# Optimization experiments

Hardware: AMD Instinct MI355X
Metric: run time of the kernel (lower is better)

Reference implementation:

```python
import jax, jax.numpy as jnp
import numpy as np

D_MODEL = 256; N_HEADS = 8; N_LEVELS = 4; N_POINTS = 4; NUM_ITER = 2
SHAPES = [(92, 160), (46, 80), (23, 40), (12, 20)]  # 4-level FPN, Len_in = 19560
LEN_IN = sum(h * w for h, w in SHAPES)
N_BATCH = 2


def _offset_bias():
    # faithful to _reset_parameters grid init of sampling_offsets.bias
    thetas = jnp.arange(N_HEADS, dtype=jnp.float32) * (2.0 * np.pi / N_HEADS)
    grid = jnp.stack([jnp.cos(thetas), jnp.sin(thetas)], -1)
    grid = grid / jnp.max(jnp.abs(grid), axis=-1, keepdims=True)
    grid = jnp.tile(grid[:, None, None, :], (1, N_LEVELS, N_POINTS, 1))
    grid = grid * (jnp.arange(N_POINTS, dtype=jnp.float32) + 1.0)[None, None, :, None]
    return grid.reshape(-1)


def setup_inputs() -> dict:
    key = jax.random.key(0)
    ks = jax.random.split(key, 12)
    N, Lq, d = N_BATCH, LEN_IN, D_MODEL
    s = 0.02
    return {
        "query0": jax.random.normal(ks[0], (N, Lq, d), jnp.float32),
        "query1": jax.random.normal(ks[1], (N, Lq, d), jnp.float32),
        "reference_points": jax.random.uniform(ks[2], (N, Lq, N_LEVELS, 2), jnp.float32),
        "input_flatten0": jax.random.normal(ks[3], (N, LEN_IN, d), jnp.float32),
        "input_flatten1": jax.random.normal(ks[4], (N, LEN_IN, d), jnp.float32),
        "input_spatial_shapes": jnp.array(SHAPES, jnp.int32),
        "input_level_start_index": jnp.array(np.cumsum([0] + [h * w for h, w in SHAPES[:-1]]), jnp.int32),
        "W_so": s * jax.random.normal(ks[5], (d, N_HEADS * N_LEVELS * N_POINTS * 2), jnp.float32),
        "b_so": _offset_bias(),
        "W_aw": s * jax.random.normal(ks[6], (d, N_HEADS * N_LEVELS * N_POINTS), jnp.float32),
        "b_aw": jnp.zeros((N_HEADS * N_LEVELS * N_POINTS,), jnp.float32),
        "W_v": s * jax.random.normal(ks[7], (d, d), jnp.float32),
        "b_v": jnp.zeros((d,), jnp.float32),
        "W_o": s * jax.random.normal(ks[8], (d, d), jnp.float32),
        "b_o": jnp.zeros((d,), jnp.float32),
        "W_agg": s * jax.random.normal(ks[9], (d * NUM_ITER, d), jnp.float32),
        "b_agg": jnp.zeros((d,), jnp.float32),
    }


def _sample_level(v_l, loc_l, H, W):
    # v_l: (N, nH, H*W, D); loc_l: (N, Lq, nH, P, 2) in [0,1]
    # bilinear, align_corners=False, zero padding (matches grid_sample fallback / CUDA kernel)
    x = loc_l[..., 0] * W - 0.5
    y = loc_l[..., 1] * H - 0.5
    x0 = jnp.floor(x); y0 = jnp.floor(y)

    def gather(xi, yi):
        inb = ((xi >= 0) & (xi <= W - 1) & (yi >= 0) & (yi <= H - 1)).astype(v_l.dtype)
        idx = (jnp.clip(yi, 0, H - 1) * W + jnp.clip(xi, 0, W - 1)).astype(jnp.int32)
        idx_t = jnp.transpose(idx, (0, 2, 1, 3))  # (N, nH, Lq, P)
        g = jax.vmap(jax.vmap(lambda vt, it: vt[it]))(v_l, idx_t)  # (N, nH, Lq, P, D)
        return g * jnp.transpose(inb, (0, 2, 1, 3))[..., None]

    def wt(w):
        return jnp.transpose(w, (0, 2, 1, 3))[..., None]

    return (wt((y0 + 1 - y) * (x0 + 1 - x)) * gather(x0, y0)
            + wt((y0 + 1 - y) * (x - x0)) * gather(x0 + 1, y0)
            + wt((y - y0) * (x0 + 1 - x)) * gather(x0, y0 + 1)
            + wt((y - y0) * (x - x0)) * gather(x0 + 1, y0 + 1))  # (N, nH, Lq, P, D)


def _ms_deform_attn(value, loc, attn, shapes, starts):
    # value: (N, Len_in, nH, D); loc: (N, Lq, nH, L, P, 2); attn: (N, Lq, nH, L, P)
    v = jnp.transpose(value, (0, 2, 1, 3))  # (N, nH, Len_in, D)
    acc = None
    for lvl in range(N_LEVELS):
        H, W = int(shapes[lvl, 0]), int(shapes[lvl, 1])
        s = int(starts[lvl])
        out_l = _sample_level(v[:, :, s:s + H * W], loc[:, :, :, lvl], H, W)
        a = jnp.transpose(attn[:, :, :, lvl], (0, 2, 1, 3))  # (N, nH, Lq, P)
        term = jnp.einsum('nhqpd,nhqp->nhqd', out_l, a)
        acc = term if acc is None else acc + term
    N, nH, Lq, D = acc.shape
    return jnp.transpose(acc, (0, 2, 1, 3)).reshape(N, Lq, nH * D)


def reference(query0, query1, reference_points, input_flatten0, input_flatten1,
              input_spatial_shapes, input_level_start_index,
              W_so, b_so, W_aw, b_aw, W_v, b_v, W_o, b_o, W_agg, b_agg):
    shapes = np.asarray(input_spatial_shapes)
    starts = np.asarray(input_level_start_index)
    N, Lq, d = query0.shape
    nH, L, P = N_HEADS, N_LEVELS, N_POINTS
    queries = [query0, query1]
    flats = [input_flatten0, input_flatten1]
    values, offs, aws = [], [], []
    for q, f in zip(queries, flats):
        values.append((f @ W_v + b_v).reshape(N, -1, nH, d // nH))
        offs.append((q @ W_so + b_so).reshape(N, Lq, nH, L, P, 2))
        aws.append((q @ W_aw + b_aw).reshape(N, Lq, nH, L * P))
    # joint softmax over num_iter * n_levels * n_points (the one-shot trick)
    aw_all = jax.nn.softmax(jnp.concatenate(aws, axis=-1), axis=-1)
    # (L, 2) normalizer = (W, H)
    normalizer = jnp.stack([input_spatial_shapes[..., 1], input_spatial_shapes[..., 0]], -1).astype(query0.dtype)
    outs = []
    for i in range(NUM_ITER):
        aw_i = aw_all[..., i * L * P:(i + 1) * L * P].reshape(N, Lq, nH, L, P)
        loc = reference_points[:, :, None, :, None, :] + offs[i] / normalizer[None, None, None, :, None, :]
        o = _ms_deform_attn(values[i], loc, aw_i, shapes, starts)
        outs.append(o @ W_o + b_o)
    return jnp.concatenate(outs, axis=-1) @ W_agg + b_agg
```

## Files before the change

kernel.cpp:

```cpp
#include <hip/hip_runtime.h>
#include <math.h>

#define NBATCH 2
#define LQ     19560
#define LEN    19560
#define NQ     (NBATCH * LQ)
#define DMODEL 256
#define NHEADS 8
#define HDIM   32
#define NLEV   4
#define NPTS   4
#define LDQS   384

typedef __bf16 bf16x8 __attribute__((ext_vector_type(8)));
typedef float  f32x4  __attribute__((ext_vector_type(4)));
typedef float  f32x2  __attribute__((ext_vector_type(2)));

__device__ inline unsigned short f2bf(float f) {
    unsigned int u = __float_as_uint(f);
    u += 0x7FFFu + ((u >> 16) & 1u);
    return (unsigned short)(u >> 16);
}
__device__ inline f32x2 bfpair(unsigned int u) {
    f32x2 r;
    r.x = __uint_as_float(u << 16);
    r.y = __uint_as_float(u & 0xFFFF0000u);
    return r;
}

__global__ __launch_bounds__(256) void prep_all(
    const float* __restrict__ q0, const float* __restrict__ q1,
    const float* __restrict__ f0, const float* __restrict__ f1,
    const float* __restrict__ Wv, const float* __restrict__ Wso,
    const float* __restrict__ Waw, const float* __restrict__ bso,
    const float* __restrict__ baw,
    const float* __restrict__ Wo, const float* __restrict__ Wagg,
    const float* __restrict__ bo, const float* __restrict__ bagg,
    unsigned short* __restrict__ Qb0, unsigned short* __restrict__ Qb1,
    unsigned short* __restrict__ Fb0, unsigned short* __restrict__ Fb1,
    unsigned short* __restrict__ Wvt, unsigned short* __restrict__ Wsoawt,
    float* __restrict__ bsoaw,
    unsigned short* __restrict__ Wfcat, float* __restrict__ bfused)
{
    const int b = blockIdx.x;
    if (b < 19560) {
        const int tsel = b / 4890;
        const int x = b - tsel * 4890;
        const float* s = (tsel & 2) ? ((tsel & 1) ? f1 : f0) : ((tsel & 1) ? q1 : q0);
        unsigned short* d = (tsel & 2) ? ((tsel & 1) ? Fb1 : Fb0) : ((tsel & 1) ? Qb1 : Qb0);
        size_t i = ((size_t)x * 256 + threadIdx.x) * 8;
        float4 a = *(const float4*)(s + i);
        float4 c = *(const float4*)(s + i + 4);
        union { uint4 u; unsigned short h[8]; } t;
        t.h[0] = f2bf(a.x); t.h[1] = f2bf(a.y); t.h[2] = f2bf(a.z); t.h[3] = f2bf(a.w);
        t.h[4] = f2bf(c.x); t.h[5] = f2bf(c.y); t.h[6] = f2bf(c.z); t.h[7] = f2bf(c.w);
        if (tsel & 2) {
            *(uint4*)(d + i) = t.u;
        } else {
            size_t row = i >> 8; int c8 = (int)(i & 255);
            *(uint4*)(d + row * 768 + 512 + c8) = t.u;
        }
    } else if (b < 19560 + 640) {
        int o = (b - 19560) * 256 + threadIdx.x;
        if (o < 65536) {
            int n = o >> 8, k = o & 255;
            Wvt[o] = f2bf(Wv[(size_t)k * 256 + n]);
        } else {
            int p = o - 65536;
            int n = p >> 8, k = p & 255;
            float v = (n < 256) ? Wso[(size_t)k * 256 + n] : Waw[(size_t)k * 128 + (n - 256)];
            Wsoawt[p] = f2bf(v);
        }
        if (o < 384) bsoaw[o] = (o < 256) ? bso[o] : baw[o - 256];
    } else {
        int k = b - 20200;
        int n = threadIdx.x;
        float s0 = 0.f, s1 = 0.f;
        for (int j = 0; j < 256; j++) {
            float w = Wo[k * 256 + j];
            s0 += w * Wagg[j * 256 + n];
            s1 += w * Wagg[(256 + j) * 256 + n];
        }
        Wfcat[(size_t)n * 512 + k]       = f2bf(s0);
        Wfcat[(size_t)n * 512 + 256 + k] = f2bf(s1);
        if (k == 0) {
            float bb = bagg[n];
            for (int j = 0; j < 256; j++)
                bb += bo[j] * (Wagg[j * 256 + n] + Wagg[(256 + j) * 256 + n]);
            bfused[n] = bb;
        }
    }
}

__global__ __launch_bounds__(256) void gemm_mega(
    const unsigned short* __restrict__ Qa0, const unsigned short* __restrict__ Qa1,
    const unsigned short* __restrict__ Fb0, const unsigned short* __restrict__ Fb1,
    const unsigned short* __restrict__ Wsoawt, const unsigned short* __restrict__ Wvt,
    const float* __restrict__ bsoaw, const float* __restrict__ bv,
    float* __restrict__ QS0, float* __restrict__ QS1,
    unsigned short* __restrict__ V0, unsigned short* __restrict__ V1,
    float* __restrict__ AW0, float* __restrict__ AW1, int awld, int zbase)
{
    const int z = blockIdx.z + zbase;
    const int isVal = (z >= 2 && z < 4);
    const int isLog = (z >= 4);
    if (isLog && blockIdx.x != 0) return;
    const int zz = z & 1;

    __shared__ __align__(16) unsigned short As[128 * 64];
    __shared__ __align__(16) unsigned short Bs[128 * 64];

    const unsigned short* A = isVal ? (zz ? Fb1 : Fb0) : (zz ? Qa1 : Qa0);
    const unsigned short* Bt = isVal ? Wvt : Wsoawt;
    const float* bias = isVal ? bv : bsoaw;
    const int lda = isVal ? 256 : 768;
    const int btrow0 = isLog ? 256 : 0;
    const int bias0 = btrow0;

    const int tid  = threadIdx.x;
    const int w    = tid >> 6, lane = tid & 63;
    const int wm = w >> 1, wn = w & 1;
    const int m0 = blockIdx.y * 128, n0 = blockIdx.x * 128;
    const int lr = lane & 15, quad = lane >> 4;

    const int sr  = lane >> 3;
    const int scl = (lane & 7) ^ sr;
    const int colb = scl * 8;
    size_t arow[4], brow[4];
    #pragma unroll
    for (int j = 0; j < 4; j++) {
        int r = (w * 4 + j) * 8 + sr;
        int ra = m0 + r; if (ra > NQ - 1) ra = NQ - 1;
        arow[j] = (size_t)ra * lda;
        brow[j] = (size_t)(btrow0 + n0 + r) * 256;
    }

    const f32x4 zero = {0.f, 0.f, 0.f, 0.f};
    f32x4 acc[4][4];
    #pragma unroll
    for (int i = 0; i < 4; i++)
        #pragma unroll
        for (int j = 0; j < 4; j++) acc[i][j] = zero;

    for (int t = 0; t < 256; t += 64) {
        #pragma unroll
        for (int j = 0; j < 4; j++) {
            int lofs = __builtin_amdgcn_readfirstlane((w * 4 + j) * 1024);
            __builtin_amdgcn_global_load_lds(
                (const __attribute__((address_space(1))) void*)(A + arow[j] + t + colb),
                (__attribute__((address_space(3))) void*)((char*)As + lofs), 16, 0, 0);
            __builtin_amdgcn_global_load_lds(
                (const __attribute__((address_space(1))) void*)(Bt + brow[j] + t + colb),
                (__attribute__((address_space(3))) void*)((char*)Bs + lofs), 16, 0, 0);
        }
        __syncthreads();

        #pragma unroll
        for (int kk = 0; kk < 2; kk++) {
            bf16x8 af[4], bff[4];
            #pragma unroll
            for (int mi = 0; mi < 4; mi++) {
                int R = wm * 64 + mi * 16 + lr;
                int pc = ((kk * 4 + quad) ^ (lr & 7)) * 16;
                af[mi] = *(const bf16x8*)((const char*)As + R * 128 + pc);
            }
            #pragma unroll
            for (int ni = 0; ni < 4; ni++) {
                int R = wn * 64 + ni * 16 + lr;
                int pc = ((kk * 4 + quad) ^ (lr & 7)) * 16;
                bff[ni] = *(const bf16x8*)((const char*)Bs + R * 128 + pc);
            }
            #pragma unroll
            for (int mi = 0; mi < 4; mi++)
                #pragma unroll
                for (int ni = 0; ni < 4; ni++)
                    acc[mi][ni] = __builtin_amdgcn_mfma_f32_16x16x32_bf16(
                        af[mi], bff[ni], acc[mi][ni], 0, 0, 0);
        }
        __syncthreads();
    }

    float* Cf = isLog ? (zz ? AW1 : AW0) : (zz ? QS1 : QS0);
    const int ldc = isLog ? awld : LDQS;
    unsigned short* Cb = zz ? V1 : V0;
    #pragma unroll
    for (int mi = 0; mi < 4; mi++) {
        #pragma unroll
        for (int reg = 0; reg < 4; reg++) {
            int row = m0 + wm * 64 + mi * 16 + quad * 4 + reg;
            if (row >= NQ) continue;
            #pragma unroll
            for (int ni = 0; ni < 4; ni++) {
                int col = n0 + wn * 64 + ni * 16 + lr;
                float v = acc[mi][ni][reg] + bias[bias0 + col];
                if (!isVal) {
                    Cf[(size_t)row * ldc + col] = v;
                } else {
                    int n = row >= LQ ? 1 : 0;
                    int pos = row - n * LQ;
                    int h = col >> 5, d = col & 31;
                    Cb[((size_t)(n * NHEADS + h) * LEN + pos) * HDIM + d] = f2bf(v);
                }
            }
        }
    }
}

#define QCHUNK 64
#define CHUNKS ((LQ + QCHUNK - 1) / QCHUNK)

__global__ __launch_bounds__(256) void ms_sample(
    const unsigned short* __restrict__ V0, const unsigned short* __restrict__ V1,
    const float* __restrict__ QS0, const float* __restrict__ QS1,
    const float* __restrict__ AW0, const float* __restrict__ AW1, int awld,
    const float* __restrict__ refp, unsigned short* __restrict__ Ocat)
{
    __shared__ unsigned int Sidx[16][65][4];
    __shared__ float        Swt [16][65][4];

    const int b = blockIdx.x;
    const int h = b & 7;
    const int rest = b >> 3;
    const int chunk = rest % CHUNKS;
    const int inn   = rest / CHUNKS;
    const int n  = inn & 1;
    const int it = inn >> 1;

    const int tid = threadIdx.x;
    const int ql  = tid >> 2;
    const int lj  = tid & 3;
    const int qraw = chunk * QCHUNK + ql;
    const bool valid = qraw < LQ;
    const int q  = valid ? qraw : LQ - 1;
    const int nq = n * LQ + q;

    const unsigned short* __restrict__ val = it ? V1 : V0;
    const float* __restrict__ QS = it ? QS1 : QS0;
    const unsigned short* __restrict__ vb2 =
        val + (size_t)(n * NHEADS + h) * LEN * HDIM;

    const int Hs[4] = {92, 46, 23, 12};
    const int Ws[4] = {160, 80, 40, 20};
    const int Ss[4] = {0, 14720, 18400, 19320};

    const float* prow = QS + (size_t)nq * LDQS;

    {
        const float4 l0 = *(const float4*)(AW0 + (size_t)nq * awld + (h << 4) + lj * 4);
        const float4 l1 = *(const float4*)(AW1 + (size_t)nq * awld + (h << 4) + lj * 4);
        float m = fmaxf(fmaxf(fmaxf(l0.x, l0.y), fmaxf(l0.z, l0.w)),
                        fmaxf(fmaxf(l1.x, l1.y), fmaxf(l1.z, l1.w)));
        m = fmaxf(m, __shfl_xor(m, 1));
        m = fmaxf(m, __shfl_xor(m, 2));
        float e0x = expf(l0.x - m), e0y = expf(l0.y - m);
        float e0z = expf(l0.z - m), e0w = expf(l0.w - m);
        float e1x = expf(l1.x - m), e1y = expf(l1.y - m);
        float e1z = expf(l1.z - m), e1w = expf(l1.w - m);
        float s = ((e0x + e0y) + (e0z + e0w)) + ((e1x + e1y) + (e1z + e1w));
        s += __shfl_xor(s, 1);
        s += __shfl_xor(s, 2);
        const float inv = 1.0f / s;
        float avs[4];
        if (it) { avs[0] = e1x * inv; avs[1] = e1y * inv; avs[2] = e1z * inv; avs[3] = e1w * inv; }
        else    { avs[0] = e0x * inv; avs[1] = e0y * inv; avs[2] = e0z * inv; avs[3] = e0w * inv; }

        const int H = Hs[lj], W = Ws[lj], S = Ss[lj];
        const float4 o0 = *(const float4*)(prow + (h << 5) + lj * 8);
        const float4 o1 = *(const float4*)(prow + (h << 5) + lj * 8 + 4);
        const float2 rp = *(const float2*)(refp + (size_t)nq * 8 + lj * 2);
        const float fx = rp.x * (float)W - 0.5f;
        const float fy = rp.y * (float)H - 0.5f;
        const float oxs[4] = {o0.x, o0.z, o1.x, o1.z};
        const float oys[4] = {o0.y, o0.w, o1.y, o1.w};
        #pragma unroll
        for (int k = 0; k < NPTS; k++) {
            const float x = fx + oxs[k];
            const float y = fy + oys[k];
            const float x0f = floorf(x), y0f = floorf(y);
            const int x0 = (int)x0f, y0 = (int)y0f;
            const float wx1 = x - x0f, wy1 = y - y0f;
            const float wx0 = 1.0f - wx1, wy0 = 1.0f - wy1;
            const int xc0 = min(max(x0, 0), W - 1);
            const int xc1 = min(max(x0 + 1, 0), W - 1);
            const int yc0 = min(max(y0, 0), H - 1);
            const int yc1 = min(max(y0 + 1, 0), H - 1);
            const float a = avs[k];
            const float ay0 = ((unsigned int)y0 < (unsigned int)H) ? a * wy0 : 0.f;
            const float ay1 = ((unsigned int)(y0 + 1) < (unsigned int)H) ? a * wy1 : 0.f;
            const float mx0 = ((unsigned int)x0 < (unsigned int)W) ? wx0 : 0.f;
            const float mx1 = ((unsigned int)(x0 + 1) < (unsigned int)W) ? wx1 : 0.f;
            const int r0 = S + yc0 * W, r1 = S + yc1 * W;
            uint4 eo4;
            eo4.x = (unsigned int)(r0 + xc0) << 5;
            eo4.y = (unsigned int)(r0 + xc1) << 5;
            eo4.z = (unsigned int)(r1 + xc0) << 5;
            eo4.w = (unsigned int)(r1 + xc1) << 5;
            *(uint4*)&Sidx[lj * 4 + k][ql][0] = eo4;
            float4 w4 = make_float4(ay0 * mx0, ay0 * mx1, ay1 * mx0, ay1 * mx1);
            *(float4*)&Swt[lj * 4 + k][ql][0] = w4;
        }
    }
    __syncthreads();

    const int dl = lj << 3;
    const unsigned short* __restrict__ vdl = vb2 + dl;

    f32x2 acc[4];
    #pragma unroll
    for (int i = 0; i < 4; i++) acc[i] = (f32x2){0.f, 0.f};

    auto corner = [&](unsigned int eo, float wgt) {
        const uint4 c = *(const uint4*)(vdl + eo);
        const f32x2 w2 = {wgt, wgt};
        acc[0] += w2 * bfpair(c.x);
        acc[1] += w2 * bfpair(c.y);
        acc[2] += w2 * bfpair(c.z);
        acc[3] += w2 * bfpair(c.w);
    };

    #pragma unroll
    for (int p = 0; p < 16; p++) {
        const uint4 i4 = *(const uint4*)&Sidx[p][ql][0];
        const float4 w4 = *(const float4*)&Swt[p][ql][0];
        corner(i4.x, w4.x);
        corner(i4.y, w4.y);
        corner(i4.z, w4.z);
        corner(i4.w, w4.w);
    }

    if (valid) {
        union { uint4 u; unsigned short s[8]; } t;
        #pragma unroll
        for (int i = 0; i < 4; i++) {
            t.s[2 * i]     = f2bf(acc[i].x);
            t.s[2 * i + 1] = f2bf(acc[i].y);
        }
        *(uint4*)&Ocat[(size_t)nq * 512 + it * 256 + h * HDIM + dl] = t.u;
    }
}

__global__ __launch_bounds__(256) void gemm_tail(
    const unsigned short* __restrict__ A, const unsigned short* __restrict__ Bt,
    const float* __restrict__ bias, float* __restrict__ C)
{
    __shared__ __align__(16) unsigned short As[128 * 64];
    __shared__ __align__(16) unsigned short Bs[128 * 64];

    const int tid  = threadIdx.x;
    const int w    = tid >> 6, lane = tid & 63;
    const int wm = w >> 1, wn = w & 1;
    const int m0 = blockIdx.y * 128, n0 = blockIdx.x * 128;
    const int lr = lane & 15, quad = lane >> 4;

    const int sr  = lane >> 3;
    const int scl = (lane & 7) ^ sr;
    const int colb = scl * 8;
    size_t arow[4], brow[4];
    #pragma unroll
    for (int j = 0; j < 4; j++) {
        int r = (w * 4 + j) * 8 + sr;
        int ra = m0 + r; if (ra > NQ - 1) ra = NQ - 1;
        arow[j] = (size_t)ra * 512;
        brow[j] = (size_t)(n0 + r) * 512;
    }

    const f32x4 zero = {0.f, 0.f, 0.f, 0.f};
    f32x4 acc[4][4];
    #pragma unroll
    for (int i = 0; i < 4; i++)
        #pragma unroll
        for (int j = 0; j < 4; j++) acc[i][j] = zero;

    for (int t = 0; t < 512; t += 64) {
        #pragma unroll
        for (int j = 0; j < 4; j++) {
            int lofs = __builtin_amdgcn_readfirstlane((w * 4 + j) * 1024);
            __builtin_amdgcn_global_load_lds(
                (const __attribute__((address_space(1))) void*)(A + arow[j] + t + colb),
                (__attribute__((address_space(3))) void*)((char*)As + lofs), 16, 0, 0);
            __builtin_amdgcn_global_load_lds(
                (const __attribute__((address_space(1))) void*)(Bt + brow[j] + t + colb),
                (__attribute__((address_space(3))) void*)((char*)Bs + lofs), 16, 0, 0);
        }
        __syncthreads();

        #pragma unroll
        for (int kk = 0; kk < 2; kk++) {
            bf16x8 af[4], bff[4];
            #pragma unroll
            for (int mi = 0; mi < 4; mi++) {
                int R = wm * 64 + mi * 16 + lr;
                int pc = ((kk * 4 + quad) ^ (lr & 7)) * 16;
                af[mi] = *(const bf16x8*)((const char*)As + R * 128 + pc);
            }
            #pragma unroll
            for (int ni = 0; ni < 4; ni++) {
                int R = wn * 64 + ni * 16 + lr;
                int pc = ((kk * 4 + quad) ^ (lr & 7)) * 16;
                bff[ni] = *(const bf16x8*)((const char*)Bs + R * 128 + pc);
            }
            #pragma unroll
            for (int mi = 0; mi < 4; mi++)
                #pragma unroll
                for (int ni = 0; ni < 4; ni++)
                    acc[mi][ni] = __builtin_amdgcn_mfma_f32_16x16x32_bf16(
                        af[mi], bff[ni], acc[mi][ni], 0, 0, 0);
        }
        __syncthreads();
    }

    #pragma unroll
    for (int mi = 0; mi < 4; mi++) {
        #pragma unroll
        for (int reg = 0; reg < 4; reg++) {
            int row = m0 + wm * 64 + mi * 16 + quad * 4 + reg;
            if (row >= NQ) continue;
            #pragma unroll
            for (int ni = 0; ni < 4; ni++) {
                int col = n0 + wn * 64 + ni * 16 + lr;
                C[(size_t)row * 256 + col] = acc[mi][ni][reg] + bias[col];
            }
        }
    }
}

extern "C" void kernel_launch(void* const* d_in, const int* in_sizes, int n_in,
                              void* d_out, int out_size, void* d_ws, size_t ws_size,
                              hipStream_t stream)
{
    const float* q0    = (const float*)d_in[0];
    const float* q1    = (const float*)d_in[1];
    const float* refp  = (const float*)d_in[2];
    const float* f0    = (const float*)d_in[3];
    const float* f1    = (const float*)d_in[4];
    const float* W_so  = (const float*)d_in[7];
    const float* b_so  = (const float*)d_in[8];
    const float* W_aw  = (const float*)d_in[9];
    const float* b_aw  = (const float*)d_in[10];
    const float* W_v   = (const float*)d_in[11];
    const float* b_v   = (const float*)d_in[12];
    const float* W_o   = (const float*)d_in[13];
    const float* b_o   = (const float*)d_in[14];
    const float* W_agg = (const float*)d_in[15];
    const float* b_agg = (const float*)d_in[16];
    float* out = (float*)d_out;

    float* ws = (float*)d_ws;
    float* QS0 = ws;
    float* QS1 = QS0 + (size_t)NQ * LDQS;
    unsigned short* V0   = (unsigned short*)(QS1 + (size_t)NQ * LDQS);
    unsigned short* V1   = V0 + (size_t)NQ * 256;
    unsigned short* Ocat = V1 + (size_t)NQ * 256;
    unsigned short* Wvt    = Ocat + (size_t)NQ * 512;
    unsigned short* Wsoawt = Wvt + 65536;
    unsigned short* Wfcat  = Wsoawt + 98304;
    float* bsoaw = (float*)(Wfcat + 131072);
    float* bfus  = bsoaw + 384;
    float* wsend = bfus + 256;

    unsigned short* Qb0 = (unsigned short*)QS0;
    unsigned short* Qb1 = (unsigned short*)QS1;
    unsigned short* Fb0 = Ocat;
    unsigned short* Fb1 = Ocat + (size_t)NQ * 256;
    const unsigned short* Qa0 = (const unsigned short*)QS0 + 512;
    const unsigned short* Qa1 = (const unsigned short*)QS1 + 512;

    size_t aw_bytes = (size_t)NQ * 128 * 4 * 2;
    size_t need_merged = ((size_t)((char*)wsend - (char*)ws)) + aw_bytes;
    const int merged = ws_size >= need_merged;
    float *AW0, *AW1;
    int awld;
    if (merged) {
        AW0 = wsend;
        AW1 = AW0 + (size_t)NQ * 128;
        awld = 128;
    } else {
        AW0 = QS0 + 256;
        AW1 = QS1 + 256;
        awld = LDQS;
    }

    const int MB = (NQ + 127) / 128;
    dim3 blk(256);

    prep_all<<<20456, blk, 0, stream>>>(
        q0, q1, f0, f1, W_v, W_so, W_aw, b_so, b_aw, W_o, W_agg, b_o, b_agg,
        Qb0, Qb1, Fb0, Fb1, Wvt, Wsoawt, bsoaw, Wfcat, bfus);

    if (merged) {
        gemm_mega<<<dim3(2, MB, 6), blk, 0, stream>>>(
            Qa0, Qa1, Fb0, Fb1, Wsoawt, Wvt, bsoaw, b_v,
            QS0, QS1, V0, V1, AW0, AW1, awld, 0);
    } else {
        gemm_mega<<<dim3(2, MB, 4), blk, 0, stream>>>(
            Qa0, Qa1, Fb0, Fb1, Wsoawt, Wvt, bsoaw, b_v,
            QS0, QS1, V0, V1, AW0, AW1, awld, 0);
        gemm_mega<<<dim3(1, MB, 2), blk, 0, stream>>>(
            Qa0, Qa1, Fb0, Fb1, Wsoawt, Wvt, bsoaw, b_v,
            QS0, QS1, V0, V1, AW0, AW1, awld, 4);
    }

    ms_sample<<<2 * 2 * CHUNKS * 8, blk, 0, stream>>>(
        V0, V1, QS0, QS1, AW0, AW1, awld, refp, Ocat);

    gemm_tail<<<dim3(2, MB, 1), blk, 0, stream>>>(Ocat, Wfcat, bfus, out);
}
```

Baseline: 474.2 us.

## Fuse joint softmax into attention-logit GEMM epilogue and pack sample indices to u16

```diff
diff --git a/kernel.cpp b/kernel.cpp
--- a/kernel.cpp
+++ b/kernel.cpp
@@ -102,20 +102,19 @@
     float* __restrict__ AW0, float* __restrict__ AW1, int awld, int zbase)
 {
     const int z = blockIdx.z + zbase;
-    const int isVal = (z >= 2 && z < 4);
-    const int isLog = (z >= 4);
+    const int isVal = (z == 2 || z == 3);
+    const int isLog = (z == 4);
     if (isLog && blockIdx.x != 0) return;
     const int zz = z & 1;
 
     __shared__ __align__(16) unsigned short As[128 * 64];
     __shared__ __align__(16) unsigned short Bs[128 * 64];
 
-    const unsigned short* A = isVal ? (zz ? Fb1 : Fb0) : (zz ? Qa1 : Qa0);
+    const unsigned short* A0p = isVal ? (zz ? Fb1 : Fb0)
+                              : (isLog ? Qa0 : (zz ? Qa1 : Qa0));
     const unsigned short* Bt = isVal ? Wvt : Wsoawt;
-    const float* bias = isVal ? bv : bsoaw;
     const int lda = isVal ? 256 : 768;
     const int btrow0 = isLog ? 256 : 0;
-    const int bias0 = btrow0;
 
     const int tid  = threadIdx.x;
     const int w    = tid >> 6, lane = tid & 63;
@@ -136,52 +135,87 @@
     }
 
     const f32x4 zero = {0.f, 0.f, 0.f, 0.f};
-    f32x4 acc[4][4];
+    f32x4 acc[4][4], acc2[4][4];
     #pragma unroll
     for (int i = 0; i < 4; i++)
         #pragma unroll
-        for (int j = 0; j < 4; j++) acc[i][j] = zero;
-
-    for (int t = 0; t < 256; t += 64) {
-        #pragma unroll
-        for (int j = 0; j < 4; j++) {
-            int lofs = __builtin_amdgcn_readfirstlane((w * 4 + j) * 1024);
-            __builtin_amdgcn_global_load_lds(
-                (const __attribute__((address_space(1))) void*)(A + arow[j] + t + colb),
-                (__attribute__((address_space(3))) void*)((char*)As + lofs), 16, 0, 0);
-            __builtin_amdgcn_global_load_lds(
-                (const __attribute__((address_space(1))) void*)(Bt + brow[j] + t + colb),
-                (__attribute__((address_space(3))) void*)((char*)Bs + lofs), 16, 0, 0);
-        }
-        __syncthreads();
-
-        #pragma unroll
-        for (int kk = 0; kk < 2; kk++) {
-            bf16x8 af[4], bff[4];
-            #pragma unroll
-            for (int mi = 0; mi < 4; mi++) {
-                int R = wm * 64 + mi * 16 + lr;
-                int pc = ((kk * 4 + quad) ^ (lr & 7)) * 16;
-                af[mi] = *(const bf16x8*)((const char*)As + R * 128 + pc);
-            }
-            #pragma unroll
-            for (int ni = 0; ni < 4; ni++) {
-                int R = wn * 64 + ni * 16 + lr;
-                int pc = ((kk * 4 + quad) ^ (lr & 7)) * 16;
-                bff[ni] = *(const bf16x8*)((const char*)Bs + R * 128 + pc);
-            }
-            #pragma unroll
-            for (int mi = 0; mi < 4; mi++)
+        for (int j = 0; j < 4; j++) { acc[i][j] = zero; acc2[i][j] = zero; }
+
+    auto kloop = [&](const unsigned short* A, f32x4 (&ac)[4][4]) {
+        for (int t = 0; t < 256; t += 64) {
+            #pragma unroll
+            for (int j = 0; j < 4; j++) {
+                int lofs = __builtin_amdgcn_readfirstlane((w * 4 + j) * 1024);
+                __builtin_amdgcn_global_load_lds(
+                    (const __attribute__((address_space(1))) void*)(A + arow[j] + t + colb),
+                    (__attribute__((address_space(3))) void*)((char*)As + lofs), 16, 0, 0);
+                __builtin_amdgcn_global_load_lds(
+                    (const __attribute__((address_space(1))) void*)(Bt + brow[j] + t + colb),
+                    (__attribute__((address_space(3))) void*)((char*)Bs + lofs), 16, 0, 0);
+            }
+            __syncthreads();
+            #pragma unroll
+            for (int kk = 0; kk < 2; kk++) {
+                bf16x8 af[4], bff[4];
                 #pragma unroll
-                for (int ni = 0; ni < 4; ni++)
-                    acc[mi][ni] = __builtin_amdgcn_mfma_f32_16x16x32_bf16(
-                        af[mi], bff[ni], acc[mi][ni], 0, 0, 0);
-        }
-        __syncthreads();
-    }
-
-    float* Cf = isLog ? (zz ? AW1 : AW0) : (zz ? QS1 : QS0);
-    const int ldc = isLog ? awld : LDQS;
+                for (int mi = 0; mi < 4; mi++) {
+                    int R = wm * 64 + mi * 16 + lr;
+                    int pc = ((kk * 4 + quad) ^ (lr & 7)) * 16;
+                    af[mi] = *(const bf16x8*)((const char*)As + R * 128 + pc);
+                }
+                #pragma unroll
+                for (int ni = 0; ni < 4; ni++) {
+                    int R = wn * 64 + ni * 16 + lr;
+                    int pc = ((kk * 4 + quad) ^ (lr & 7)) * 16;
+                    bff[ni] = *(const bf16x8*)((const char*)Bs + R * 128 + pc);
+                }
+                #pragma unroll
+                for (int mi = 0; mi < 4; mi++)
+                    #pragma unroll
+                    for (int ni = 0; ni < 4; ni++)
+                        ac[mi][ni] = __builtin_amdgcn_mfma_f32_16x16x32_bf16(
+                            af[mi], bff[ni], ac[mi][ni], 0, 0, 0);
+            }
+            __syncthreads();
+        }
+    };
+
+    kloop(A0p, acc);
+    if (isLog) kloop(Qa1, acc2);
+
+    if (isLog) {
+        float bvv[4];
+        #pragma unroll
+        for (int ni = 0; ni < 4; ni++) bvv[ni] = bsoaw[256 + wn * 64 + ni * 16 + lr];
+        #pragma unroll
+        for (int mi = 0; mi < 4; mi++) {
+            #pragma unroll
+            for (int reg = 0; reg < 4; reg++) {
+                int row = m0 + wm * 64 + mi * 16 + quad * 4 + reg;
+                #pragma unroll
+                for (int ni = 0; ni < 4; ni++) {
+                    float a = acc[mi][ni][reg] + bvv[ni];
+                    float c = acc2[mi][ni][reg] + bvv[ni];
+                    float m = fmaxf(a, c);
+                    #pragma unroll
+                    for (int d = 1; d < 16; d <<= 1) m = fmaxf(m, __shfl_xor(m, d));
+                    float ea = expf(a - m), ec = expf(c - m);
+                    float s = ea + ec;
+                    #pragma unroll
+                    for (int d = 1; d < 16; d <<= 1) s += __shfl_xor(s, d);
+                    float inv = 1.0f / s;
+                    if (row < NQ) {
+                        int col = wn * 64 + ni * 16 + lr;
+                        AW0[(size_t)row * awld + col] = ea * inv;
+                        AW1[(size_t)row * awld + col] = ec * inv;
+                    }
+                }
+            }
+        }
+        return;
+    }
+
+    float* Cf = zz ? QS1 : QS0;
     unsigned short* Cb = zz ? V1 : V0;
     #pragma unroll
     for (int mi = 0; mi < 4; mi++) {
@@ -192,10 +226,10 @@
             #pragma unroll
             for (int ni = 0; ni < 4; ni++) {
                 int col = n0 + wn * 64 + ni * 16 + lr;
-                float v = acc[mi][ni][reg] + bias[bias0 + col];
                 if (!isVal) {
-                    Cf[(size_t)row * ldc + col] = v;
+                    Cf[(size_t)row * LDQS + col] = acc[mi][ni][reg] + bsoaw[col];
                 } else {
+                    float v = acc[mi][ni][reg] + bv[col];
                     int n = row >= LQ ? 1 : 0;
                     int pos = row - n * LQ;
                     int h = col >> 5, d = col & 31;
@@ -215,8 +249,8 @@
     const float* __restrict__ AW0, const float* __restrict__ AW1, int awld,
     const float* __restrict__ refp, unsigned short* __restrict__ Ocat)
 {
-    __shared__ unsigned int Sidx[16][65][4];
-    __shared__ float        Swt [16][65][4];
+    __shared__ unsigned short Sidx[16][65][4];
+    __shared__ float          Swt [16][65][4];
 
     const int b = blockIdx.x;
     const int h = b & 7;
@@ -236,6 +270,7 @@
 
     const unsigned short* __restrict__ val = it ? V1 : V0;
     const float* __restrict__ QS = it ? QS1 : QS0;
+    const float* __restrict__ AW = it ? AW1 : AW0;
     const unsigned short* __restrict__ vb2 =
         val + (size_t)(n * NHEADS + h) * LEN * HDIM;
 
@@ -246,32 +281,16 @@
     const float* prow = QS + (size_t)nq * LDQS;
 
     {
-        const float4 l0 = *(const float4*)(AW0 + (size_t)nq * awld + (h << 4) + lj * 4);
-        const float4 l1 = *(const float4*)(AW1 + (size_t)nq * awld + (h << 4) + lj * 4);
-        float m = fmaxf(fmaxf(fmaxf(l0.x, l0.y), fmaxf(l0.z, l0.w)),
-                        fmaxf(fmaxf(l1.x, l1.y), fmaxf(l1.z, l1.w)));
-        m = fmaxf(m, __shfl_xor(m, 1));
-        m = fmaxf(m, __shfl_xor(m, 2));
-        float e0x = expf(l0.x - m), e0y = expf(l0.y - m);
-        float e0z = expf(l0.z - m), e0w = expf(l0.w - m);
-        float e1x = expf(l1.x - m), e1y = expf(l1.y - m);
-        float e1z = expf(l1.z - m), e1w = expf(l1.w - m);
-        float s = ((e0x + e0y) + (e0z + e0w)) + ((e1x + e1y) + (e1z + e1w));
-        s += __shfl_xor(s, 1);
-        s += __shfl_xor(s, 2);
-        const float inv = 1.0f / s;
-        float avs[4];
-        if (it) { avs[0] = e1x * inv; avs[1] = e1y * inv; avs[2] = e1z * inv; avs[3] = e1w * inv; }
-        else    { avs[0] = e0x * inv; avs[1] = e0y * inv; avs[2] = e0z * inv; avs[3] = e0w * inv; }
-
         const int H = Hs[lj], W = Ws[lj], S = Ss[lj];
         const float4 o0 = *(const float4*)(prow + (h << 5) + lj * 8);
         const float4 o1 = *(const float4*)(prow + (h << 5) + lj * 8 + 4);
+        const float4 a4 = *(const float4*)(AW + (size_t)nq * awld + (h << 4) + lj * 4);
         const float2 rp = *(const float2*)(refp + (size_t)nq * 8 + lj * 2);
         const float fx = rp.x * (float)W - 0.5f;
         const float fy = rp.y * (float)H - 0.5f;
         const float oxs[4] = {o0.x, o0.z, o1.x, o1.z};
         const float oys[4] = {o0.y, o0.w, o1.y, o1.w};
+        const float avs[4] = {a4.x, a4.y, a4.z, a4.w};
         #pragma unroll
         for (int k = 0; k < NPTS; k++) {
             const float x = fx + oxs[k];
@@ -290,12 +309,12 @@
             const float mx0 = ((unsigned int)x0 < (unsigned int)W) ? wx0 : 0.f;
             const float mx1 = ((unsigned int)(x0 + 1) < (unsigned int)W) ? wx1 : 0.f;
             const int r0 = S + yc0 * W, r1 = S + yc1 * W;
-            uint4 eo4;
-            eo4.x = (unsigned int)(r0 + xc0) << 5;
-            eo4.y = (unsigned int)(r0 + xc1) << 5;
-            eo4.z = (unsigned int)(r1 + xc0) << 5;
-            eo4.w = (unsigned int)(r1 + xc1) << 5;
-            *(uint4*)&Sidx[lj * 4 + k][ql][0] = eo4;
+            union { uint2 u; unsigned short s4[4]; } ip;
+            ip.s4[0] = (unsigned short)(r0 + xc0);
+            ip.s4[1] = (unsigned short)(r0 + xc1);
+            ip.s4[2] = (unsigned short)(r1 + xc0);
+            ip.s4[3] = (unsigned short)(r1 + xc1);
+            *(uint2*)&Sidx[lj * 4 + k][ql][0] = ip.u;
             float4 w4 = make_float4(ay0 * mx0, ay0 * mx1, ay1 * mx0, ay1 * mx1);
             *(float4*)&Swt[lj * 4 + k][ql][0] = w4;
         }
@@ -320,12 +339,12 @@
 
     #pragma unroll
     for (int p = 0; p < 16; p++) {
-        const uint4 i4 = *(const uint4*)&Sidx[p][ql][0];
+        const uint2 i2 = *(const uint2*)&Sidx[p][ql][0];
         const float4 w4 = *(const float4*)&Swt[p][ql][0];
-        corner(i4.x, w4.x);
-        corner(i4.y, w4.y);
-        corner(i4.z, w4.z);
-        corner(i4.w, w4.w);
+        corner((i2.x & 0xFFFFu) << 5, w4.x);
+        corner((i2.x >> 16) << 5, w4.y);
+        corner((i2.y & 0xFFFFu) << 5, w4.z);
+        corner((i2.y >> 16) << 5, w4.w);
     }
 
     if (valid) {
@@ -488,14 +507,14 @@
         Qb0, Qb1, Fb0, Fb1, Wvt, Wsoawt, bsoaw, Wfcat, bfus);
 
     if (merged) {
-        gemm_mega<<<dim3(2, MB, 6), blk, 0, stream>>>(
+        gemm_mega<<<dim3(2, MB, 5), blk, 0, stream>>>(
             Qa0, Qa1, Fb0, Fb1, Wsoawt, Wvt, bsoaw, b_v,
             QS0, QS1, V0, V1, AW0, AW1, awld, 0);
     } else {
         gemm_mega<<<dim3(2, MB, 4), blk, 0, stream>>>(
             Qa0, Qa1, Fb0, Fb1, Wsoawt, Wvt, bsoaw, b_v,
             QS0, QS1, V0, V1, AW0, AW1, awld, 0);
-        gemm_mega<<<dim3(1, MB, 2), blk, 0, stream>>>(
+        gemm_mega<<<dim3(1, MB, 1), blk, 0, stream>>>(
             Qa0, Qa1, Fb0, Fb1, Wsoawt, Wvt, bsoaw, b_v,
             QS0, QS1, V0, V1, AW0, AW1, awld, 4);
     }
```

Result: slower. 544.2 us (+14.8%).
